# Kernel optimization log

Measured on AMD Instinct MI355X. Metric: run time of the kernel, lower is better.

## Reference

```python
import jax, jax.numpy as jnp
import numpy as np

N_NODES = 50000
N_EDGES = 600000
F_IN = 128
F_OUT = 128
N_RELS = 8


def setup_inputs() -> dict:
    key = jax.random.key(0)
    k1, k2, k3, k4, k5 = jax.random.split(key, 5)
    X = jax.random.normal(k1, (N_NODES, F_IN), dtype=jnp.float32)
    W = jax.random.normal(k2, (N_RELS, F_OUT, F_IN), dtype=jnp.float32) * (1.0 / np.sqrt(F_IN))
    edge_src = jax.random.randint(k3, (N_EDGES,), 0, N_NODES, dtype=jnp.int32)
    edge_dst = jax.random.randint(k4, (N_EDGES,), 0, N_NODES, dtype=jnp.int32)
    edge_type = jax.random.randint(k5, (N_EDGES,), 0, N_RELS, dtype=jnp.int32)
    return {
        "X": X,
        "W": W,
        "edge_src": edge_src,
        "edge_dst": edge_dst,
        "edge_type": edge_type,
        "num_nodes": N_NODES,
    }


def reference(X, W, edge_src, edge_dst, edge_type, num_nodes):
    # RGCN hetero forward: Y[i, fo] = sum_{edges (j->i) of relation r} W[r, fo, fi] * X[j, fi]
    # Transform all node features by every relation's weight (dense GEMM, high intensity):
    # H[r, n, fo] = sum_fi W[r, fo, fi] * X[n, fi]
    H = jnp.einsum("nf,rof->rno", X, W)  # [R, N, F_out]
    # Gather per-edge messages (relation-specific transformed source feature)
    msgs = H[edge_type, edge_src]  # [E, F_out]
    # Scatter-add messages to destination nodes (the atomic accumulation in the kernel)
    Y = jax.ops.segment_sum(msgs, edge_dst, num_segments=num_nodes)  # [N, F_out]
    return Y
```

## Files before the change

kernel.cpp:

```cpp
#include <hip/hip_runtime.h>

#define F 128
#define RELS 8
#define KMAX 64
#define NT 16

typedef __attribute__((ext_vector_type(8))) short short8;
typedef __attribute__((ext_vector_type(4))) float floatx4;

__device__ __forceinline__ unsigned short f2bf(float f) {
    unsigned int u = __float_as_uint(f);
    unsigned int r = (u + 0x7fffu + ((u >> 16) & 1u)) >> 16;
    return (unsigned short)r;
}

__global__ void cvtX_kernel(const float* __restrict__ X, unsigned short* __restrict__ X2, int N) {
    int t = blockIdx.x * blockDim.x + threadIdx.x;
    if (t >= N * (F / 8)) return;
    int n = t >> 4;
    int q = t & 15;
    int fi = q * 8;
    const float* xp = X + (size_t)n * F + fi;
    float4 v0 = *reinterpret_cast<const float4*>(xp);
    float4 v1 = *reinterpret_cast<const float4*>(xp + 4);
    short8 o;
    o[0] = (short)f2bf(v0.x); o[1] = (short)f2bf(v0.y);
    o[2] = (short)f2bf(v0.z); o[3] = (short)f2bf(v0.w);
    o[4] = (short)f2bf(v1.x); o[5] = (short)f2bf(v1.y);
    o[6] = (short)f2bf(v1.z); o[7] = (short)f2bf(v1.w);
    *reinterpret_cast<short8*>(X2 + (size_t)n * F + fi) = o;
}

__global__ void cvtW_kernel(const float* __restrict__ W, unsigned short* __restrict__ W2) {
    int t = blockIdx.x * blockDim.x + threadIdx.x;
    if (t >= RELS * F * (F / 8)) return;
    int r = t >> 11;
    int rem = t & 2047;
    int fo = rem >> 4;
    int q = rem & 15;
    int fi = q * 8;
    const float* wp = W + ((size_t)r * F + fo) * F + fi;
    float4 v0 = *reinterpret_cast<const float4*>(wp);
    float4 v1 = *reinterpret_cast<const float4*>(wp + 4);
    int kc = fi >> 5;
    int ko = fi & 31;
    short8 o;
    o[0] = (short)f2bf(v0.x); o[1] = (short)f2bf(v0.y);
    o[2] = (short)f2bf(v0.z); o[3] = (short)f2bf(v0.w);
    o[4] = (short)f2bf(v1.x); o[5] = (short)f2bf(v1.y);
    o[6] = (short)f2bf(v1.z); o[7] = (short)f2bf(v1.w);
    *reinterpret_cast<short8*>(W2 + ((size_t)((r * 4 + kc) * F + fo)) * 32 + ko) = o;
}

__global__ void fillp_kernel(const int* __restrict__ src, const int* __restrict__ dst,
                             const int* __restrict__ et, int* __restrict__ counts,
                             unsigned int* __restrict__ packed, int E) {
    int t = blockIdx.x * blockDim.x + threadIdx.x;
    if (t >= E) return;
    int d = dst[t];
    int slot = atomicAdd(&counts[d], 1);
    if (slot < KMAX)
        packed[(size_t)d * KMAX + slot] = (unsigned int)src[t] | ((unsigned int)et[t] << 24);
}

#define LOF(v) __uint_as_float((v) << 16)
#define HIF(v) __uint_as_float((v) & 0xffff0000u)
#define ACC(rr, vv)                                                        \
    {                                                                      \
        unsigned int _r = (rr);                                            \
        unsigned int _v = (vv);                                            \
        switch (_r) {                                                      \
            case 0: a0x += LOF(_v); a0y += HIF(_v); break;                 \
            case 1: a1x += LOF(_v); a1y += HIF(_v); break;                 \
            case 2: a2x += LOF(_v); a2y += HIF(_v); break;                 \
            case 3: a3x += LOF(_v); a3y += HIF(_v); break;                 \
            case 4: a4x += LOF(_v); a4y += HIF(_v); break;                 \
            case 5: a5x += LOF(_v); a5y += HIF(_v); break;                 \
            case 6: a6x += LOF(_v); a6y += HIF(_v); break;                 \
            default: a7x += LOF(_v); a7y += HIF(_v); break;                \
        }                                                                  \
    }

__global__ __launch_bounds__(256) void fused_kernel(const unsigned int* __restrict__ X2u,
                                                    const unsigned short* __restrict__ W2,
                                                    const int* __restrict__ counts,
                                                    const unsigned int* __restrict__ packed,
                                                    float* __restrict__ Y, int N) {
    __shared__ unsigned int Zl[RELS * NT * 64];
    int lane = threadIdx.x & 63;
    int wave = threadIdx.x >> 6;
    int nodebase = blockIdx.x * NT;

#pragma unroll 1
    for (int i = 0; i < NT / 4; i++) {
        int nl = wave * (NT / 4) + i;
        int node = nodebase + nl;
        float a0x = 0, a0y = 0, a1x = 0, a1y = 0, a2x = 0, a2y = 0, a3x = 0, a3y = 0;
        float a4x = 0, a4y = 0, a5x = 0, a5y = 0, a6x = 0, a6y = 0, a7x = 0, a7y = 0;
        if (node < N) {
            int cnt = counts[node];
            if (cnt > KMAX) cnt = KMAX;
            const unsigned int* pk = packed + (size_t)node * KMAX;
            int nq = cnt >> 2;
            int rem = cnt & 3;
            if (nq) {
                uint4 p = *reinterpret_cast<const uint4*>(pk);
#pragma unroll 1
                for (int qi = 1; qi < nq; qi++) {
                    uint4 pn = *reinterpret_cast<const uint4*>(pk + qi * 4);
                    unsigned int v0 = X2u[(size_t)(p.x & 0xffffffu) * 64 + lane];
                    unsigned int v1 = X2u[(size_t)(p.y & 0xffffffu) * 64 + lane];
                    unsigned int v2 = X2u[(size_t)(p.z & 0xffffffu) * 64 + lane];
                    unsigned int v3 = X2u[(size_t)(p.w & 0xffffffu) * 64 + lane];
                    ACC(p.x >> 24, v0);
                    ACC(p.y >> 24, v1);
                    ACC(p.z >> 24, v2);
                    ACC(p.w >> 24, v3);
                    p = pn;
                }
                unsigned int v0 = X2u[(size_t)(p.x & 0xffffffu) * 64 + lane];
                unsigned int v1 = X2u[(size_t)(p.y & 0xffffffu) * 64 + lane];
                unsigned int v2 = X2u[(size_t)(p.z & 0xffffffu) * 64 + lane];
                unsigned int v3 = X2u[(size_t)(p.w & 0xffffffu) * 64 + lane];
                ACC(p.x >> 24, v0);
                ACC(p.y >> 24, v1);
                ACC(p.z >> 24, v2);
                ACC(p.w >> 24, v3);
            }
            const unsigned int* tail = pk + nq * 4;
            for (int t = 0; t < rem; t++) {
                unsigned int p = tail[t];
                unsigned int v = X2u[(size_t)(p & 0xffffffu) * 64 + lane];
                ACC(p >> 24, v);
            }
        }
        int sl = lane ^ ((nl & 7) << 2);
        Zl[(0 * NT + nl) * 64 + sl] = (unsigned int)f2bf(a0x) | ((unsigned int)f2bf(a0y) << 16);
        Zl[(1 * NT + nl) * 64 + sl] = (unsigned int)f2bf(a1x) | ((unsigned int)f2bf(a1y) << 16);
        Zl[(2 * NT + nl) * 64 + sl] = (unsigned int)f2bf(a2x) | ((unsigned int)f2bf(a2y) << 16);
        Zl[(3 * NT + nl) * 64 + sl] = (unsigned int)f2bf(a3x) | ((unsigned int)f2bf(a3y) << 16);
        Zl[(4 * NT + nl) * 64 + sl] = (unsigned int)f2bf(a4x) | ((unsigned int)f2bf(a4y) << 16);
        Zl[(5 * NT + nl) * 64 + sl] = (unsigned int)f2bf(a5x) | ((unsigned int)f2bf(a5y) << 16);
        Zl[(6 * NT + nl) * 64 + sl] = (unsigned int)f2bf(a6x) | ((unsigned int)f2bf(a6y) << 16);
        Zl[(7 * NT + nl) * 64 + sl] = (unsigned int)f2bf(a7x) | ((unsigned int)f2bf(a7y) << 16);
    }
    __syncthreads();

    int lr = lane & 15;
    int hi = lane >> 4;
    int lk8 = hi * 8;
    int nl0 = lr;
    floatx4 acc00 = {0, 0, 0, 0}, acc01 = {0, 0, 0, 0};
#pragma unroll
    for (int r = 0; r < RELS; r++) {
#pragma unroll
        for (int kc = 0; kc < 4; kc++) {
            int ks = kc * 16 + hi * 4;
            short8 av = *reinterpret_cast<const short8*>(&Zl[(r * NT + nl0) * 64 + (ks ^ ((nl0 & 7) << 2))]);
            short8 b0 = *reinterpret_cast<const short8*>(W2 + ((size_t)((r * 4 + kc) * F + (wave * 2) * 16 + lr)) * 32 + lk8);
            short8 b1 = *reinterpret_cast<const short8*>(W2 + ((size_t)((r * 4 + kc) * F + (wave * 2 + 1) * 16 + lr)) * 32 + lk8);
            acc00 = __builtin_amdgcn_mfma_f32_16x16x32_bf16(av, b0, acc00, 0, 0, 0);
            acc01 = __builtin_amdgcn_mfma_f32_16x16x32_bf16(av, b1, acc01, 0, 0, 0);
        }
    }

    int c0 = (wave * 2) * 16 + lr;
    int c1 = (wave * 2 + 1) * 16 + lr;
#pragma unroll
    for (int g = 0; g < 4; g++) {
        int row = nodebase + hi * 4 + g;
        if (row < N) {
            Y[(size_t)row * F + c0] = acc00[g];
            Y[(size_t)row * F + c1] = acc01[g];
        }
    }
}

__global__ void fused_fb_kernel(const float* __restrict__ X, const float* __restrict__ W,
                                const int* __restrict__ src, const int* __restrict__ dst,
                                const int* __restrict__ et, float* __restrict__ Y, int E) {
    int lane = threadIdx.x & 63;
    int wid = (blockIdx.x * blockDim.x + threadIdx.x) >> 6;
    int nw = (gridDim.x * blockDim.x) >> 6;
    for (int e = wid; e < E; e += nw) {
        int s = src[e];
        int d = dst[e];
        int r = et[e];
        const float4* xr = reinterpret_cast<const float4*>(X + (size_t)s * F);
#pragma unroll
        for (int h = 0; h < 2; h++) {
            int fo = lane + (h << 6);
            const float4* wr = reinterpret_cast<const float4*>(W + ((size_t)r * F + fo) * F);
            float acc = 0.f;
#pragma unroll
            for (int i = 0; i < 32; i++) {
                float4 x = xr[i];
                float4 w = wr[i];
                acc += x.x * w.x + x.y * w.y + x.z * w.z + x.w * w.w;
            }
            unsafeAtomicAdd(&Y[(size_t)d * F + fo], acc);
        }
    }
}

extern "C" void kernel_launch(void* const* d_in, const int* in_sizes, int n_in,
                              void* d_out, int out_size, void* d_ws, size_t ws_size,
                              hipStream_t stream) {
    const float* X = (const float*)d_in[0];
    const float* W = (const float*)d_in[1];
    const int* src = (const int*)d_in[2];
    const int* dst = (const int*)d_in[3];
    const int* et  = (const int*)d_in[4];
    int N = in_sizes[0] / F;
    int E = in_sizes[2];
    float* Y = (float*)d_out;

    size_t x2bytes  = (size_t)N * F * 2;
    size_t w2bytes  = (size_t)RELS * F * F * 2;
    size_t cntbytes = ((size_t)N * 4 + 255) & ~255ull;
    size_t pkbytes  = (size_t)N * KMAX * 4;
    size_t need = x2bytes + w2bytes + cntbytes + pkbytes;

    if (ws_size < need) {
        hipMemsetAsync(d_out, 0, (size_t)N * F * sizeof(float), stream);
        fused_fb_kernel<<<2048, 256, 0, stream>>>(X, W, src, dst, et, Y, E);
        return;
    }

    char* ws = (char*)d_ws;
    unsigned short* X2 = (unsigned short*)ws;  ws += x2bytes;
    unsigned short* W2 = (unsigned short*)ws;  ws += w2bytes;
    int* counts        = (int*)ws;             ws += cntbytes;
    unsigned int* packed = (unsigned int*)ws;

    hipMemsetAsync(counts, 0, (size_t)N * 4, stream);
    fillp_kernel<<<(E + 255) / 256, 256, 0, stream>>>(src, dst, et, counts, packed, E);

    cvtX_kernel<<<(N * (F / 8) + 255) / 256, 256, 0, stream>>>(X, X2, N);
    cvtW_kernel<<<(RELS * F * (F / 8) + 255) / 256, 256, 0, stream>>>(W, W2);

    fused_kernel<<<(N + NT - 1) / NT, 256, 0, stream>>>((const unsigned int*)X2, W2, counts, packed, Y, N);
}
```

Baseline: 220.1 us.

## Merge prep kernels into one launch and accumulate relation sums via LDS atomics

The three preprocessing kernels (edge bucketing, X and W bf16 conversion) become one launch that picks its role from the block index, which saves two kernel launches. The fused kernel now runs 512 threads with 8 waves. It accumulates per-relation sums in an fp32 LDS buffer with shared-memory atomics instead of a switch over 16 register accumulators, and each wave computes one 16-column MFMA tile. This removes the divergent switch and register pressure, but adds LDS atomic traffic, a zeroing pass, and a larger 64KB LDS footprint that may limit occupancy.

New measurement: 570.2 us. 2.59x slower.

```diff
diff --git a/kernel.cpp b/kernel.cpp
--- a/kernel.cpp
+++ b/kernel.cpp
@@ -14,93 +14,91 @@
     return (unsigned short)r;
 }
 
-__global__ void cvtX_kernel(const float* __restrict__ X, unsigned short* __restrict__ X2, int N) {
-    int t = blockIdx.x * blockDim.x + threadIdx.x;
-    if (t >= N * (F / 8)) return;
-    int n = t >> 4;
-    int q = t & 15;
-    int fi = q * 8;
-    const float* xp = X + (size_t)n * F + fi;
-    float4 v0 = *reinterpret_cast<const float4*>(xp);
-    float4 v1 = *reinterpret_cast<const float4*>(xp + 4);
-    short8 o;
-    o[0] = (short)f2bf(v0.x); o[1] = (short)f2bf(v0.y);
-    o[2] = (short)f2bf(v0.z); o[3] = (short)f2bf(v0.w);
-    o[4] = (short)f2bf(v1.x); o[5] = (short)f2bf(v1.y);
-    o[6] = (short)f2bf(v1.z); o[7] = (short)f2bf(v1.w);
-    *reinterpret_cast<short8*>(X2 + (size_t)n * F + fi) = o;
-}
-
-__global__ void cvtW_kernel(const float* __restrict__ W, unsigned short* __restrict__ W2) {
-    int t = blockIdx.x * blockDim.x + threadIdx.x;
-    if (t >= RELS * F * (F / 8)) return;
-    int r = t >> 11;
-    int rem = t & 2047;
-    int fo = rem >> 4;
-    int q = rem & 15;
-    int fi = q * 8;
-    const float* wp = W + ((size_t)r * F + fo) * F + fi;
-    float4 v0 = *reinterpret_cast<const float4*>(wp);
-    float4 v1 = *reinterpret_cast<const float4*>(wp + 4);
-    int kc = fi >> 5;
-    int ko = fi & 31;
-    short8 o;
-    o[0] = (short)f2bf(v0.x); o[1] = (short)f2bf(v0.y);
-    o[2] = (short)f2bf(v0.z); o[3] = (short)f2bf(v0.w);
-    o[4] = (short)f2bf(v1.x); o[5] = (short)f2bf(v1.y);
-    o[6] = (short)f2bf(v1.z); o[7] = (short)f2bf(v1.w);
-    *reinterpret_cast<short8*>(W2 + ((size_t)((r * 4 + kc) * F + fo)) * 32 + ko) = o;
-}
-
-__global__ void fillp_kernel(const int* __restrict__ src, const int* __restrict__ dst,
-                             const int* __restrict__ et, int* __restrict__ counts,
-                             unsigned int* __restrict__ packed, int E) {
-    int t = blockIdx.x * blockDim.x + threadIdx.x;
-    if (t >= E) return;
-    int d = dst[t];
-    int slot = atomicAdd(&counts[d], 1);
-    if (slot < KMAX)
-        packed[(size_t)d * KMAX + slot] = (unsigned int)src[t] | ((unsigned int)et[t] << 24);
-}
-
 #define LOF(v) __uint_as_float((v) << 16)
 #define HIF(v) __uint_as_float((v) & 0xffff0000u)
-#define ACC(rr, vv)                                                        \
-    {                                                                      \
-        unsigned int _r = (rr);                                            \
-        unsigned int _v = (vv);                                            \
-        switch (_r) {                                                      \
-            case 0: a0x += LOF(_v); a0y += HIF(_v); break;                 \
-            case 1: a1x += LOF(_v); a1y += HIF(_v); break;                 \
-            case 2: a2x += LOF(_v); a2y += HIF(_v); break;                 \
-            case 3: a3x += LOF(_v); a3y += HIF(_v); break;                 \
-            case 4: a4x += LOF(_v); a4y += HIF(_v); break;                 \
-            case 5: a5x += LOF(_v); a5y += HIF(_v); break;                 \
-            case 6: a6x += LOF(_v); a6y += HIF(_v); break;                 \
-            default: a7x += LOF(_v); a7y += HIF(_v); break;                \
-        }                                                                  \
-    }
-
-__global__ __launch_bounds__(256) void fused_kernel(const unsigned int* __restrict__ X2u,
+
+__global__ __launch_bounds__(256) void prep_kernel(const float* __restrict__ X, const float* __restrict__ W,
+                                                   const int* __restrict__ src, const int* __restrict__ dst,
+                                                   const int* __restrict__ et,
+                                                   unsigned short* __restrict__ X2, unsigned short* __restrict__ W2,
+                                                   int* __restrict__ counts, unsigned int* __restrict__ packed,
+                                                   int E, int N, int BF, int BX) {
+    int bid = blockIdx.x;
+    int tid = threadIdx.x;
+    if (bid < BF) {
+        int t = bid * 256 + tid;
+        if (t < E) {
+            int d = dst[t];
+            int slot = atomicAdd(&counts[d], 1);
+            if (slot < KMAX)
+                packed[(size_t)d * KMAX + slot] = (unsigned int)src[t] | ((unsigned int)et[t] << 24);
+        }
+    } else if (bid < BF + BX) {
+        int t = (bid - BF) * 256 + tid;
+        if (t < N * (F / 8)) {
+            int n = t >> 4;
+            int fi = (t & 15) * 8;
+            const float* xp = X + (size_t)n * F + fi;
+            float4 v0 = *reinterpret_cast<const float4*>(xp);
+            float4 v1 = *reinterpret_cast<const float4*>(xp + 4);
+            short8 o;
+            o[0] = (short)f2bf(v0.x); o[1] = (short)f2bf(v0.y);
+            o[2] = (short)f2bf(v0.z); o[3] = (short)f2bf(v0.w);
+            o[4] = (short)f2bf(v1.x); o[5] = (short)f2bf(v1.y);
+            o[6] = (short)f2bf(v1.z); o[7] = (short)f2bf(v1.w);
+            *reinterpret_cast<short8*>(X2 + (size_t)n * F + fi) = o;
+        }
+    } else {
+        int t = (bid - BF - BX) * 256 + tid;
+        if (t < RELS * F * (F / 8)) {
+            int r = t >> 11;
+            int rem = t & 2047;
+            int fo = rem >> 4;
+            int fi = (rem & 15) * 8;
+            const float* wp = W + ((size_t)r * F + fo) * F + fi;
+            float4 v0 = *reinterpret_cast<const float4*>(wp);
+            float4 v1 = *reinterpret_cast<const float4*>(wp + 4);
+            int kc = fi >> 5;
+            int ko = fi & 31;
+            short8 o;
+            o[0] = (short)f2bf(v0.x); o[1] = (short)f2bf(v0.y);
+            o[2] = (short)f2bf(v0.z); o[3] = (short)f2bf(v0.w);
+            o[4] = (short)f2bf(v1.x); o[5] = (short)f2bf(v1.y);
+            o[6] = (short)f2bf(v1.z); o[7] = (short)f2bf(v1.w);
+            *reinterpret_cast<short8*>(W2 + ((size_t)((r * 4 + kc) * F + fo)) * 32 + ko) = o;
+        }
+    }
+}
+
+__global__ __launch_bounds__(512) void fused_kernel(const unsigned int* __restrict__ X2u,
                                                     const unsigned short* __restrict__ W2,
                                                     const int* __restrict__ counts,
                                                     const unsigned int* __restrict__ packed,
                                                     float* __restrict__ Y, int N) {
-    __shared__ unsigned int Zl[RELS * NT * 64];
-    int lane = threadIdx.x & 63;
-    int wave = threadIdx.x >> 6;
+    __shared__ float Zf[NT * RELS * F];
+    int tid = threadIdx.x;
+    int lane = tid & 63;
+    int wave = tid >> 6;
     int nodebase = blockIdx.x * NT;
 
+    float4* zp = reinterpret_cast<float4*>(Zf);
+#pragma unroll
+    for (int i = 0; i < 8; i++) zp[i * 512 + tid] = make_float4(0.f, 0.f, 0.f, 0.f);
+    __syncthreads();
+
+    int k0 = 2 * lane;
 #pragma unroll 1
-    for (int i = 0; i < NT / 4; i++) {
-        int nl = wave * (NT / 4) + i;
+    for (int i = 0; i < 2; i++) {
+        int nl = wave * 2 + i;
         int node = nodebase + nl;
-        float a0x = 0, a0y = 0, a1x = 0, a1y = 0, a2x = 0, a2y = 0, a3x = 0, a3y = 0;
-        float a4x = 0, a4y = 0, a5x = 0, a5y = 0, a6x = 0, a6y = 0, a7x = 0, a7y = 0;
         if (node < N) {
             int cnt = counts[node];
             if (cnt > KMAX) cnt = KMAX;
             const unsigned int* pk = packed + (size_t)node * KMAX;
+            int sw = (nl & 7) << 2;
+            int i0 = k0 ^ sw;
+            int i1 = (k0 + 1) ^ sw;
+            float* zrow = Zf + (size_t)nl * (RELS * F);
             int nq = cnt >> 2;
             int rem = cnt & 3;
             if (nq) {
@@ -112,67 +110,68 @@
                     unsigned int v1 = X2u[(size_t)(p.y & 0xffffffu) * 64 + lane];
                     unsigned int v2 = X2u[(size_t)(p.z & 0xffffffu) * 64 + lane];
                     unsigned int v3 = X2u[(size_t)(p.w & 0xffffffu) * 64 + lane];
-                    ACC(p.x >> 24, v0);
-                    ACC(p.y >> 24, v1);
-                    ACC(p.z >> 24, v2);
-                    ACC(p.w >> 24, v3);
+                    float* z0 = zrow + (p.x >> 24) * F;
+                    atomicAdd(z0 + i0, LOF(v0)); atomicAdd(z0 + i1, HIF(v0));
+                    float* z1 = zrow + (p.y >> 24) * F;
+                    atomicAdd(z1 + i0, LOF(v1)); atomicAdd(z1 + i1, HIF(v1));
+                    float* z2 = zrow + (p.z >> 24) * F;
+                    atomicAdd(z2 + i0, LOF(v2)); atomicAdd(z2 + i1, HIF(v2));
+                    float* z3 = zrow + (p.w >> 24) * F;
+                    atomicAdd(z3 + i0, LOF(v3)); atomicAdd(z3 + i1, HIF(v3));
                     p = pn;
                 }
                 unsigned int v0 = X2u[(size_t)(p.x & 0xffffffu) * 64 + lane];
                 unsigned int v1 = X2u[(size_t)(p.y & 0xffffffu) * 64 + lane];
                 unsigned int v2 = X2u[(size_t)(p.z & 0xffffffu) * 64 + lane];
                 unsigned int v3 = X2u[(size_t)(p.w & 0xffffffu) * 64 + lane];
-                ACC(p.x >> 24, v0);
-                ACC(p.y >> 24, v1);
-                ACC(p.z >> 24, v2);
-                ACC(p.w >> 24, v3);
+                float* z0 = zrow + (p.x >> 24) * F;
+                atomicAdd(z0 + i0, LOF(v0)); atomicAdd(z0 + i1, HIF(v0));
+                float* z1 = zrow + (p.y >> 24) * F;
+                atomicAdd(z1 + i0, LOF(v1)); atomicAdd(z1 + i1, HIF(v1));
+                float* z2 = zrow + (p.z >> 24) * F;
+                atomicAdd(z2 + i0, LOF(v2)); atomicAdd(z2 + i1, HIF(v2));
+                float* z3 = zrow + (p.w >> 24) * F;
+                atomicAdd(z3 + i0, LOF(v3)); atomicAdd(z3 + i1, HIF(v3));
             }
             const unsigned int* tail = pk + nq * 4;
             for (int t = 0; t < rem; t++) {
                 unsigned int p = tail[t];
                 unsigned int v = X2u[(size_t)(p & 0xffffffu) * 64 + lane];
-                ACC(p >> 24, v);
+                float* z = zrow + (p >> 24) * F;
+                atomicAdd(z + i0, LOF(v)); atomicAdd(z + i1, HIF(v));
             }
         }
-        int sl = lane ^ ((nl & 7) << 2);
-        Zl[(0 * NT + nl) * 64 + sl] = (unsigned int)f2bf(a0x) | ((unsigned int)f2bf(a0y) << 16);
-        Zl[(1 * NT + nl) * 64 + sl] = (unsigned int)f2bf(a1x) | ((unsigned int)f2bf(a1y) << 16);
-        Zl[(2 * NT + nl) * 64 + sl] = (unsigned int)f2bf(a2x) | ((unsigned int)f2bf(a2y) << 16);
-        Zl[(3 * NT + nl) * 64 + sl] = (unsigned int)f2bf(a3x) | ((unsigned int)f2bf(a3y) << 16);
-        Zl[(4 * NT + nl) * 64 + sl] = (unsigned int)f2bf(a4x) | ((unsigned int)f2bf(a4y) << 16);
-        Zl[(5 * NT + nl) * 64 + sl] = (unsigned int)f2bf(a5x) | ((unsigned int)f2bf(a5y) << 16);
-        Zl[(6 * NT + nl) * 64 + sl] = (unsigned int)f2bf(a6x) | ((unsigned int)f2bf(a6y) << 16);
-        Zl[(7 * NT + nl) * 64 + sl] = (unsigned int)f2bf(a7x) | ((unsigned int)f2bf(a7y) << 16);
     }
     __syncthreads();
 
     int lr = lane & 15;
     int hi = lane >> 4;
-    int lk8 = hi * 8;
-    int nl0 = lr;
-    floatx4 acc00 = {0, 0, 0, 0}, acc01 = {0, 0, 0, 0};
+    int sw = (lr & 7) << 2;
+    const float* zrow = Zf + (size_t)lr * (RELS * F);
+    floatx4 acc = {0.f, 0.f, 0.f, 0.f};
 #pragma unroll
     for (int r = 0; r < RELS; r++) {
 #pragma unroll
         for (int kc = 0; kc < 4; kc++) {
-            int ks = kc * 16 + hi * 4;
-            short8 av = *reinterpret_cast<const short8*>(&Zl[(r * NT + nl0) * 64 + (ks ^ ((nl0 & 7) << 2))]);
-            short8 b0 = *reinterpret_cast<const short8*>(W2 + ((size_t)((r * 4 + kc) * F + (wave * 2) * 16 + lr)) * 32 + lk8);
-            short8 b1 = *reinterpret_cast<const short8*>(W2 + ((size_t)((r * 4 + kc) * F + (wave * 2 + 1) * 16 + lr)) * 32 + lk8);
-            acc00 = __builtin_amdgcn_mfma_f32_16x16x32_bf16(av, b0, acc00, 0, 0, 0);
-            acc01 = __builtin_amdgcn_mfma_f32_16x16x32_bf16(av, b1, acc01, 0, 0, 0);
-        }
-    }
-
-    int c0 = (wave * 2) * 16 + lr;
-    int c1 = (wave * 2 + 1) * 16 + lr;
+            int kbase = kc * 32 + hi * 8;
+            float4 f0 = *reinterpret_cast<const float4*>(zrow + r * F + (kbase ^ sw));
+            float4 f1 = *reinterpret_cast<const float4*>(zrow + r * F + ((kbase + 4) ^ sw));
+            uint4 uu;
+            asm("v_cvt_pk_bf16_f32 %0, %1, %2" : "=v"(uu.x) : "v"(f0.x), "v"(f0.y));
+            asm("v_cvt_pk_bf16_f32 %0, %1, %2" : "=v"(uu.y) : "v"(f0.z), "v"(f0.w));
+            asm("v_cvt_pk_bf16_f32 %0, %1, %2" : "=v"(uu.z) : "v"(f1.x), "v"(f1.y));
+            asm("v_cvt_pk_bf16_f32 %0, %1, %2" : "=v"(uu.w) : "v"(f1.z), "v"(f1.w));
+            short8 av = *reinterpret_cast<short8*>(&uu);
+            short8 b = *reinterpret_cast<const short8*>(W2 + ((size_t)((r * 4 + kc) * F + wave * 16 + lr)) * 32 + hi * 8);
+            acc = __builtin_amdgcn_mfma_f32_16x16x32_bf16(av, b, acc, 0, 0, 0);
+        }
+    }
+
+    int col = wave * 16 + lr;
 #pragma unroll
     for (int g = 0; g < 4; g++) {
         int row = nodebase + hi * 4 + g;
-        if (row < N) {
-            Y[(size_t)row * F + c0] = acc00[g];
-            Y[(size_t)row * F + c1] = acc01[g];
-        }
+        if (row < N) Y[(size_t)row * F + col] = acc[g];
     }
 }
 
@@ -233,11 +232,11 @@
     int* counts        = (int*)ws;             ws += cntbytes;
     unsigned int* packed = (unsigned int*)ws;
 
+    int BF = (E + 255) / 256;
+    int BX = (N * (F / 8) + 255) / 256;
+    int BW = (RELS * F * (F / 8) + 255) / 256;
+
     hipMemsetAsync(counts, 0, (size_t)N * 4, stream);
-    fillp_kernel<<<(E + 255) / 256, 256, 0, stream>>>(src, dst, et, counts, packed, E);
-
-    cvtX_kernel<<<(N * (F / 8) + 255) / 256, 256, 0, stream>>>(X, X2, N);
-    cvtW_kernel<<<(RELS * F * (F / 8) + 255) / 256, 256, 0, stream>>>(W, W2);
-
-    fused_kernel<<<(N + NT - 1) / NT, 256, 0, stream>>>((const unsigned int*)X2, W2, counts, packed, Y, N);
-}
+    prep_kernel<<<BF + BX + BW, 256, 0, stream>>>(X, W, src, dst, et, X2, W2, counts, packed, E, N, BF, BX);
+    fused_kernel<<<(N + NT - 1) / NT, 512, 0, stream>>>((const unsigned int*)X2, W2, counts, packed, Y, N);
+}
```
